# Optimization experiments

Measured on AMD Instinct MI355X. Metric: run time of the kernel, lower is better.

The kernel has to match this reference:

```python
import jax, jax.numpy as jnp
import numpy as np

B, D, N, H, K = 8192, 1024, 4096, 8, 4
T, DECAY, STEPS = 100.0, 0.001, 3


def setup_inputs() -> dict:
    key = jax.random.key(0)
    ks = jax.random.split(key, 16)
    rn = lambda k, sh, s=0.02: jax.random.normal(k, sh, jnp.float32) * s
    return {
        'query': jax.random.normal(ks[0], (B, D), jnp.float32),
        'wm': jax.random.normal(ks[1], (B, D), jnp.float32),
        'keys': jax.random.normal(ks[2], (N, D), jnp.float32) * 0.1,
        'values': jax.random.normal(ks[3], (N, D), jnp.float32) * 0.1,
        'last_access': jax.random.uniform(ks[4], (N,), jnp.float32) * T,
        'importance': jnp.ones((N,), jnp.float32),
        'consolid': jnp.ones((N,), jnp.float32),
        'emo_tags': jax.random.uniform(ks[5], (N, 8), jnp.float32),
        'active': jnp.ones((N,), jnp.float32),
        'in_proj_w': rn(ks[6], (3 * D, D)), 'in_proj_b': jnp.zeros((3 * D,), jnp.float32),
        'out_w': rn(ks[7], (D, D)), 'out_b': jnp.zeros((D,), jnp.float32),
        'msg_w1': rn(ks[8], (D, 2 * D)), 'msg_b1': jnp.zeros((D,), jnp.float32),
        'msg_ln_g': jnp.ones((D,), jnp.float32), 'msg_ln_b': jnp.zeros((D,), jnp.float32),
        'msg_w2': rn(ks[9], (D, D)), 'msg_b2': jnp.zeros((D,), jnp.float32),
        'gru_wih': rn(ks[10], (3 * D, D)), 'gru_whh': rn(ks[11], (3 * D, D)),
        'gru_bih': jnp.zeros((3 * D,), jnp.float32), 'gru_bhh': jnp.zeros((3 * D,), jnp.float32),
        'rsn_w1': rn(ks[12], (D, D)), 'rsn_b1': jnp.zeros((D,), jnp.float32),
        'rsn_ln_g': jnp.ones((D,), jnp.float32), 'rsn_ln_b': jnp.zeros((D,), jnp.float32),
        'rsn_w2': rn(ks[13], (D, D)), 'rsn_b2': jnp.zeros((D,), jnp.float32),
        'top_k': K,
    }


def _ln(x, g, b):
    m = x.mean(-1, keepdims=True)
    v = ((x - m) ** 2).mean(-1, keepdims=True)
    return (x - m) / jnp.sqrt(v + 1e-5) * g + b


def reference(query, wm, keys, values, last_access, importance, consolid, emo_tags, active,
              in_proj_w, in_proj_b, out_w, out_b,
              msg_w1, msg_b1, msg_ln_g, msg_ln_b, msg_w2, msg_b2,
              gru_wih, gru_whh, gru_bih, gru_bhh,
              rsn_w1, rsn_b1, rsn_ln_g, rsn_ln_b, rsn_w2, rsn_b2, top_k):
    sg = jax.lax.stop_gradient
    # --- schema retrieve: cosine sim + forgetting-decay + boosts + topk softmax gather ---
    qn = query / jnp.maximum(jnp.linalg.norm(query, axis=-1, keepdims=True), 1e-8)
    kn = keys / jnp.maximum(jnp.linalg.norm(keys, axis=-1, keepdims=True), 1e-8)
    sims = qn @ kn.T  # [B, N]
    forget = sg(jnp.exp(-DECAY * (T - last_access)))
    boost = sg(emo_tags.sum(-1) * 0.1 + importance * 0.2 + jnp.log1p(consolid) * 0.1)
    scores = (sims * forget + boost) * sg(active)
    top_s, top_i = jax.lax.top_k(scores, top_k)  # [B, K]
    w = jax.nn.softmax(top_s, axis=-1)
    schema = jnp.einsum('bk,bkd->bd', w, values[top_i])  # [B, D]

    # --- GraphReasoner: 3 steps of 2-token MHA + msg_net + GRUCell ---
    dh = D // H
    scale = 1.0 / np.sqrt(dh).astype(np.float32)

    def mha(x):  # x [B, 2, D]
        qkv = x @ in_proj_w.T + in_proj_b
        q, k, v = jnp.split(qkv, 3, axis=-1)
        q = q.reshape(-1, 2, H, dh); k = k.reshape(-1, 2, H, dh); v = v.reshape(-1, 2, H, dh)
        a = jax.nn.softmax(jnp.einsum('bqhd,bkhd->bhqk', q, k) * scale, axis=-1)
        o = jnp.einsum('bhqk,bkhd->bqhd', a, v).reshape(-1, 2, D)
        return o @ out_w.T + out_b

    def gru(x, h):
        gi = x @ gru_wih.T + gru_bih
        gh = h @ gru_whh.T + gru_bhh
        ir, iz, inn = jnp.split(gi, 3, axis=-1)
        hr, hz, hn = jnp.split(gh, 3, axis=-1)
        r = jax.nn.sigmoid(ir + hr)
        z = jax.nn.sigmoid(iz + hz)
        n = jnp.tanh(inn + r * hn)
        return (1.0 - z) * n + z * h

    state = wm
    for _ in range(STEPS):
        ctx = jnp.stack([state, schema], axis=1)  # [B, 2, D]
        att = mha(ctx)
        combined = jnp.concatenate([att[:, 0], att[:, 1]], axis=-1)  # [B, 2D]
        msg = jax.nn.relu(_ln(combined @ msg_w1.T + msg_b1, msg_ln_g, msg_ln_b)) @ msg_w2.T + msg_b2
        state = gru(msg, state)
    out = jax.nn.relu(_ln(state @ rsn_w1.T + rsn_b1, rsn_ln_g, rsn_ln_b)) @ rsn_w2.T + rsn_b2
    return out
```

## Files before the change

### kernel.cpp

```cpp
#include <hip/hip_runtime.h>
#include <cstdint>
#include <cstddef>

typedef __attribute__((ext_vector_type(8))) short short8;
typedef __attribute__((ext_vector_type(4))) float f32x4;
typedef __attribute__((ext_vector_type(4))) unsigned short us4;

#define DEVINL static __device__ __forceinline__
#define AS1 __attribute__((address_space(1)))
#define AS3 __attribute__((address_space(3)))

DEVINL float bf2f(unsigned short u){
  union { unsigned uu; float f; } v; v.uu = ((unsigned)u) << 16; return v.f;
}
DEVINL unsigned short f2bf(float f){
  unsigned u = __float_as_uint(f);
  u += 0x7fffu + ((u >> 16) & 1u);
  return (unsigned short)(u >> 16);
}

DEVINL bool tk_better(float av, int ai, float bv, int bi){
  return (av > bv) || (av == bv && ai < bi);
}
DEVINL void tk_cmpex(float& va, int& ia, float& vb, int& ib){
  if (!tk_better(va, ia, vb, ib)){
    float tv = va; va = vb; vb = tv;
    int t = ia; ia = ib; ib = t;
  }
}
DEVINL void tk_sort4(float* v, int* id){
  tk_cmpex(v[0], id[0], v[1], id[1]);
  tk_cmpex(v[2], id[2], v[3], id[3]);
  tk_cmpex(v[0], id[0], v[2], id[2]);
  tk_cmpex(v[1], id[1], v[3], id[3]);
  tk_cmpex(v[1], id[1], v[2], id[2]);
}
DEVINL void tk_bmerge(float* v, int* id, const float* pv, const int* pi){
  #pragma unroll
  for (int i = 0; i < 4; ++i){
    bool ta = tk_better(v[i], id[i], pv[3 - i], pi[3 - i]);
    v[i]  = ta ? v[i]  : pv[3 - i];
    id[i] = ta ? id[i] : pi[3 - i];
  }
  tk_cmpex(v[0], id[0], v[2], id[2]);
  tk_cmpex(v[1], id[1], v[3], id[3]);
  tk_cmpex(v[0], id[0], v[1], id[1]);
  tk_cmpex(v[2], id[2], v[3], id[3]);
}

__global__ void k_diag(float* out, float v){ out[0] = v; }

__global__ __launch_bounds__(256) void k_cast_bf16(const float* __restrict__ x,
                                                   unsigned short* __restrict__ y, int n4){
  int stride = gridDim.x * blockDim.x;
  for (int i = blockIdx.x * blockDim.x + threadIdx.x; i < n4; i += stride){
    float4 v = ((const float4*)x)[i];
    us4 o; o[0] = f2bf(v.x); o[1] = f2bf(v.y); o[2] = f2bf(v.z); o[3] = f2bf(v.w);
    ((us4*)y)[i] = o;
  }
}

__global__ __launch_bounds__(256) void k_tcast(const float* __restrict__ in,
    unsigned short* __restrict__ outT, int R, int C){
  __shared__ float t[32][33];
  const int bc = blockIdx.x * 32, br = blockIdx.y * 32;
  const int lx = threadIdx.x & 31, ly = threadIdx.x >> 5;
  #pragma unroll
  for (int i = 0; i < 32; i += 8)
    t[ly + i][lx] = in[(size_t)(br + ly + i) * C + bc + lx];
  __syncthreads();
  #pragma unroll
  for (int i = 0; i < 32; i += 8)
    outT[(size_t)(bc + ly + i) * R + br + lx] = f2bf(t[lx][ly + i]);
}

__global__ __launch_bounds__(256) void k_bias_pre(const float* __restrict__ w1,
    const float* __restrict__ outb, const float* __restrict__ b1, float* __restrict__ bc){
  int wave = threadIdx.x >> 6, lane = threadIdx.x & 63;
  int j = blockIdx.x * 4 + wave;
  float s = 0.f;
  for (int m = lane; m < 2048; m += 64)
    s += w1[(size_t)j * 2048 + m] * outb[m & 1023];
  #pragma unroll
  for (int m = 32; m >= 1; m >>= 1) s += __shfl_xor(s, m);
  if (lane == 0) bc[j] = s + b1[j];
}

__global__ __launch_bounds__(256) void k_bias_gi(const float* __restrict__ wih,
    const float* __restrict__ b2, const float* __restrict__ bih, float* __restrict__ bc){
  int wave = threadIdx.x >> 6, lane = threadIdx.x & 63;
  int n = blockIdx.x * 4 + wave;
  float s = 0.f;
  for (int m = lane; m < 1024; m += 64)
    s += wih[(size_t)n * 1024 + m] * b2[m];
  #pragma unroll
  for (int m = 32; m >= 1; m >>= 1) s += __shfl_xor(s, m);
  if (lane == 0) bc[n] = s + bih[n];
}

__global__ __launch_bounds__(256) void k_prep_keys(const float* __restrict__ keys,
    const float* __restrict__ last_access, const float* __restrict__ importance,
    const float* __restrict__ consolid, const float* __restrict__ emo,
    const float* __restrict__ active, float* __restrict__ ascale, float* __restrict__ bbias){
  int wave = threadIdx.x >> 6, lane = threadIdx.x & 63;
  int n = blockIdx.x * 4 + wave;
  const float* kr = keys + (size_t)n * 1024;
  float s = 0.f;
  #pragma unroll
  for (int j = 0; j < 4; ++j){
    float4 v = ((const float4*)kr)[j * 64 + lane];
    s += v.x*v.x + v.y*v.y + v.z*v.z + v.w*v.w;
  }
  #pragma unroll
  for (int m = 32; m >= 1; m >>= 1) s += __shfl_xor(s, m);
  if (lane == 0){
    float norm = fmaxf(sqrtf(s), 1e-8f);
    float forget = expf(-0.001f * (100.0f - last_access[n]));
    float bo = 0.f;
    #pragma unroll
    for (int j = 0; j < 8; ++j) bo += emo[n * 8 + j];
    bo = bo * 0.1f + importance[n] * 0.2f + log1pf(consolid[n]) * 0.1f;
    float a = active[n];
    ascale[n] = forget * a / norm;
    bbias[n]  = bo * a;
  }
}

__global__ __launch_bounds__(256) void k_qnorm(const float* __restrict__ q, float* __restrict__ qinv){
  int wave = threadIdx.x >> 6, lane = threadIdx.x & 63;
  int b = blockIdx.x * 4 + wave;
  const float* qr = q + (size_t)b * 1024;
  float s = 0.f;
  #pragma unroll
  for (int j = 0; j < 4; ++j){
    float4 v = ((const float4*)qr)[j * 64 + lane];
    s += v.x*v.x + v.y*v.y + v.z*v.z + v.w*v.w;
  }
  #pragma unroll
  for (int m = 32; m >= 1; m >>= 1) s += __shfl_xor(s, m);
  if (lane == 0) qinv[b] = 1.0f / fmaxf(sqrtf(s), 1e-8f);
}

__global__ __launch_bounds__(256) void k_split(const float* __restrict__ X,
    const float* __restrict__ rscale, unsigned short* __restrict__ Hi,
    unsigned short* __restrict__ Lo){
  const int row = blockIdx.x;
  const float sc = rscale ? rscale[row] : 1.0f;
  const int d = threadIdx.x * 4;
  float4 v = *(const float4*)(X + (size_t)row * 1024 + d);
  float xs[4] = {v.x * sc, v.y * sc, v.z * sc, v.w * sc};
  us4 h, l;
  #pragma unroll
  for (int j = 0; j < 4; ++j){
    unsigned short hb = f2bf(xs[j]);
    h[j] = hb;
    l[j] = f2bf(xs[j] - bf2f(hb));
  }
  *(us4*)(Hi + (size_t)row * 1024 + d) = h;
  *(us4*)(Lo + (size_t)row * 1024 + d) = l;
}

__global__ __launch_bounds__(256) void k_scores_mfma(
    const unsigned short* __restrict__ Qhi, const unsigned short* __restrict__ Qlo,
    const unsigned short* __restrict__ Khi, const unsigned short* __restrict__ Klo,
    const float* __restrict__ ascale, const float* __restrict__ bbias,
    float* __restrict__ candV, int* __restrict__ candI){
  __shared__ __align__(16) unsigned short AsH[128 * 32];
  __shared__ __align__(16) unsigned short AsL[128 * 32];
  __shared__ __align__(16) unsigned short BsH[128 * 32];
  __shared__ __align__(16) unsigned short BsL[128 * 32];
  const int tid = threadIdx.x;
  const int wave = tid >> 6, lane = tid & 63;
  const int tM = blockIdx.x, tN = blockIdx.y;
  const int wm_ = wave >> 1, wn_ = wave & 1;
  f32x4 acc[4][4] = {};
  const unsigned short* AH = Qhi + (size_t)tM * 128 * 1024;
  const unsigned short* AL = Qlo + (size_t)tM * 128 * 1024;
  const unsigned short* BH = Khi + (size_t)tN * 128 * 1024;
  const unsigned short* BL = Klo + (size_t)tN * 128 * 1024;
  const int lrow = lane & 15, lk = (lane >> 4) * 8;
  for (int k0 = 0; k0 < 1024; k0 += 32){
    __syncthreads();
    #pragma unroll
    for (int j = 0; j < 2; ++j){
      int c = wave * 128 + j * 64 + lane;
      int row = c >> 2, cp = c & 3;
      size_t go = (size_t)row * 1024 + k0 + cp * 8;
      int lo_ = (wave * 2 + j) * 512;
      __builtin_amdgcn_global_load_lds((const AS1 void*)(AH + go), (AS3 void*)(AsH + lo_), 16, 0, 0);
      __builtin_amdgcn_global_load_lds((const AS1 void*)(AL + go), (AS3 void*)(AsL + lo_), 16, 0, 0);
      __builtin_amdgcn_global_load_lds((const AS1 void*)(BH + go), (AS3 void*)(BsH + lo_), 16, 0, 0);
      __builtin_amdgcn_global_load_lds((const AS1 void*)(BL + go), (AS3 void*)(BsL + lo_), 16, 0, 0);
    }
    __syncthreads();
    short8 ah[4], al[4], bh[4], bl[4];
    #pragma unroll
    for (int mi = 0; mi < 4; ++mi){
      int ro = (wm_ * 64 + mi * 16 + lrow) * 32 + lk;
      ah[mi] = *(const short8*)(AsH + ro);
      al[mi] = *(const short8*)(AsL + ro);
    }
    #pragma unroll
    for (int ni = 0; ni < 4; ++ni){
      int ro = (wn_ * 64 + ni * 16 + lrow) * 32 + lk;
      bh[ni] = *(const short8*)(BsH + ro);
      bl[ni] = *(const short8*)(BsL + ro);
    }
    #pragma unroll
    for (int mi = 0; mi < 4; ++mi)
      #pragma unroll
      for (int ni = 0; ni < 4; ++ni){
        acc[mi][ni] = __builtin_amdgcn_mfma_f32_16x16x32_bf16(ah[mi], bh[ni], acc[mi][ni], 0, 0, 0);
        acc[mi][ni] = __builtin_amdgcn_mfma_f32_16x16x32_bf16(ah[mi], bl[ni], acc[mi][ni], 0, 0, 0);
        acc[mi][ni] = __builtin_amdgcn_mfma_f32_16x16x32_bf16(al[mi], bh[ni], acc[mi][ni], 0, 0, 0);
      }
  }
  const int lc = lane & 15;
  float as_[4], bb_[4]; int cid[4];
  #pragma unroll
  for (int ni = 0; ni < 4; ++ni){
    cid[ni] = tN * 128 + wn_ * 64 + ni * 16 + lc;
    as_[ni] = ascale[cid[ni]];
    bb_[ni] = bbias[cid[ni]];
  }
  #pragma unroll
  for (int mi = 0; mi < 4; ++mi){
    #pragma unroll
    for (int r = 0; r < 4; ++r){
      float v[4]; int id[4];
      #pragma unroll
      for (int ni = 0; ni < 4; ++ni){
        v[ni]  = acc[mi][ni][r] * as_[ni] + bb_[ni];
        id[ni] = cid[ni];
      }
      tk_sort4(v, id);
      #pragma unroll
      for (int mask = 1; mask <= 8; mask <<= 1){
        float pv[4]; int pi_[4];
        #pragma unroll
        for (int j = 0; j < 4; ++j){
          pv[j]  = __shfl_xor(v[j], mask);
          pi_[j] = __shfl_xor(id[j], mask);
        }
        tk_bmerge(v, id, pv, pi_);
      }
      if (lc == 0){
        int row = tM * 128 + wm_ * 64 + mi * 16 + (lane >> 4) * 4 + r;
        size_t cb = (size_t)row * 256 + tN * 8 + wn_ * 4;
        #pragma unroll
        for (int j = 0; j < 4; ++j){ candV[cb + j] = v[j]; candI[cb + j] = id[j]; }
      }
    }
  }
}

__global__ __launch_bounds__(256) void k_topk_merge(const float* __restrict__ candV,
    const int* __restrict__ candI, const float* __restrict__ V,
    unsigned short* __restrict__ schema_bf){
  const int row = blockIdx.x, tid = threadIdx.x;
  const int wave = tid >> 6, lane = tid & 63;
  float v[4]; int id[4];
  v[0] = candV[(size_t)row * 256 + tid];
  id[0] = candI[(size_t)row * 256 + tid];
  #pragma unroll
  for (int j = 1; j < 4; ++j){ v[j] = -3.4e38f; id[j] = 0x7fffffff; }
  #pragma unroll
  for (int mask = 1; mask <= 32; mask <<= 1){
    float pv[4]; int pi_[4];
    #pragma unroll
    for (int j = 0; j < 4; ++j){
      pv[j]  = __shfl_xor(v[j], mask);
      pi_[j] = __shfl_xor(id[j], mask);
    }
    tk_bmerge(v, id, pv, pi_);
  }
  __shared__ float wv[4][4]; __shared__ int wi[4][4];
  if (lane == 0){
    #pragma unroll
    for (int j = 0; j < 4; ++j){ wv[wave][j] = v[j]; wi[wave][j] = id[j]; }
  }
  __syncthreads();
  __shared__ float w_sh[4]; __shared__ int i_sh[4];
  if (tid == 0){
    float fv[4]; int fi[4];
    #pragma unroll
    for (int j = 0; j < 4; ++j){ fv[j] = wv[0][j]; fi[j] = wi[0][j]; }
    #pragma unroll
    for (int w = 1; w < 4; ++w){
      float pv[4]; int pi_[4];
      #pragma unroll
      for (int j = 0; j < 4; ++j){ pv[j] = wv[w][j]; pi_[j] = wi[w][j]; }
      tk_bmerge(fv, fi, pv, pi_);
    }
    float m = fv[0];
    float e0 = expf(fv[0] - m), e1 = expf(fv[1] - m), e2 = expf(fv[2] - m), e3 = expf(fv[3] - m);
    float inv = 1.f / (e0 + e1 + e2 + e3);
    w_sh[0] = e0 * inv; w_sh[1] = e1 * inv; w_sh[2] = e2 * inv; w_sh[3] = e3 * inv;
    i_sh[0] = fi[0]; i_sh[1] = fi[1]; i_sh[2] = fi[2]; i_sh[3] = fi[3];
  }
  __syncthreads();
  float w0 = w_sh[0], w1 = w_sh[1], w2 = w_sh[2], w3 = w_sh[3];
  const float* v0 = V + (size_t)i_sh[0] * 1024;
  const float* v1 = V + (size_t)i_sh[1] * 1024;
  const float* v2 = V + (size_t)i_sh[2] * 1024;
  const float* v3 = V + (size_t)i_sh[3] * 1024;
  int d = tid * 4;
  float4 a = *(const float4*)(v0 + d);
  float4 b4 = *(const float4*)(v1 + d);
  float4 c = *(const float4*)(v2 + d);
  float4 e = *(const float4*)(v3 + d);
  us4 o;
  o[0] = f2bf(w0*a.x + w1*b4.x + w2*c.x + w3*e.x);
  o[1] = f2bf(w0*a.y + w1*b4.y + w2*c.y + w3*e.y);
  o[2] = f2bf(w0*a.z + w1*b4.z + w2*c.z + w3*e.z);
  o[3] = f2bf(w0*a.w + w1*b4.w + w2*c.w + w3*e.w);
  *(us4*)(schema_bf + (size_t)row * 1024 + d) = o;
}

__global__ __launch_bounds__(256) void k_initstate(const float* __restrict__ wm,
    float* __restrict__ st, unsigned short* __restrict__ stbf){
  size_t i = ((size_t)blockIdx.x * 256 + threadIdx.x) * 4;
  float4 v = *(const float4*)(wm + i);
  *(float4*)(st + i) = v;
  us4 o; o[0] = f2bf(v.x); o[1] = f2bf(v.y); o[2] = f2bf(v.z); o[3] = f2bf(v.w);
  *(us4*)(stbf + i) = o;
}

template<int OUT_BF16>
__global__ __launch_bounds__(256) void k_gemm(const unsigned short* __restrict__ A,
    const unsigned short* __restrict__ W, const float* __restrict__ bias,
    void* __restrict__ C, int M, int N, int K, int lda, int ldc){
  __shared__ __align__(16) unsigned short As[128 * 32];
  __shared__ __align__(16) unsigned short Ws[128 * 32];
  const int tid = threadIdx.x;
  const int wave = tid >> 6, lane = tid & 63;
  const int tM = blockIdx.x, tN = blockIdx.y;
  const int wm_ = wave >> 1, wn_ = wave & 1;
  f32x4 acc[4][4] = {};
  const unsigned short* Abase = A + (size_t)tM * 128 * lda;
  const unsigned short* Wbase = W + (size_t)tN * 128 * K;
  const int lrow = lane & 15, lk = (lane >> 4) * 8;
  for (int k0 = 0; k0 < K; k0 += 32){
    __syncthreads();
    #pragma unroll
    for (int j = 0; j < 2; ++j){
      int c = wave * 128 + j * 64 + lane;
      int row = c >> 2, cp = c & 3;
      const unsigned short* ga = Abase + (size_t)row * lda + k0 + cp * 8;
      const unsigned short* gw = Wbase + (size_t)row * K + k0 + cp * 8;
      __builtin_amdgcn_global_load_lds((const AS1 void*)ga, (AS3 void*)(As + (wave * 2 + j) * 512), 16, 0, 0);
      __builtin_amdgcn_global_load_lds((const AS1 void*)gw, (AS3 void*)(Ws + (wave * 2 + j) * 512), 16, 0, 0);
    }
    __syncthreads();
    short8 af[4], bfr[4];
    #pragma unroll
    for (int mi = 0; mi < 4; ++mi)
      af[mi] = *(const short8*)(As + (wm_ * 64 + mi * 16 + lrow) * 32 + lk);
    #pragma unroll
    for (int ni = 0; ni < 4; ++ni)
      bfr[ni] = *(const short8*)(Ws + (wn_ * 64 + ni * 16 + lrow) * 32 + lk);
    #pragma unroll
    for (int mi = 0; mi < 4; ++mi)
      #pragma unroll
      for (int ni = 0; ni < 4; ++ni)
        acc[mi][ni] = __builtin_amdgcn_mfma_f32_16x16x32_bf16(af[mi], bfr[ni], acc[mi][ni], 0, 0, 0);
  }
  const int lc = lane & 15, lr = (lane >> 4) * 4;
  #pragma unroll
  for (int ni = 0; ni < 4; ++ni){
    int col = tN * 128 + wn_ * 64 + ni * 16 + lc;
    float bb = bias ? bias[col] : 0.f;
    #pragma unroll
    for (int mi = 0; mi < 4; ++mi){
      int rowb = tM * 128 + wm_ * 64 + mi * 16 + lr;
      #pragma unroll
      for (int r = 0; r < 4; ++r){
        float vv = acc[mi][ni][r] + bb;
        size_t off = (size_t)(rowb + r) * ldc + col;
        if (OUT_BF16) ((unsigned short*)C)[off] = f2bf(vv);
        else ((float*)C)[off] = vv;
      }
    }
  }
}

template<int OUT_BF16>
__global__ __launch_bounds__(512, 2) void k_gemm8p(const unsigned short* __restrict__ A,
    const unsigned short* __restrict__ W, const float* __restrict__ bias,
    void* __restrict__ C, int M, int N, int K, int lda, int ldc){
  __shared__ __align__(16) unsigned short lds[65536];
  const int tid = threadIdx.x;
  const int wave = tid >> 6, lane = tid & 63;
  const int wqr = wave >> 2, wqc = wave & 3;
  const int lrow = lane & 15, lkk = lane >> 4;

  const int nwg = gridDim.x * gridDim.y;
  int lin = blockIdx.y * gridDim.x + blockIdx.x;
  int cpx = nwg >> 3;
  int swz = (lin & 7) * cpx + (lin >> 3);
  const int nM = M >> 8;
  const int tM = swz % nM, tN = swz / nM;

  const unsigned short* Abase = A + (size_t)tM * 256 * lda;
  const unsigned short* Wbase = W + (size_t)tN * 256 * K;

  f32x4 a00[4][2] = {}, a01[4][2] = {}, a11[4][2] = {}, a10[4][2] = {};
  short8 af[4][2], bf[2][2];
  const int ntiles = K >> 6;

  auto stage = [&](int op, int slot, int half, int tile){
    if (tile >= ntiles) return;
    const unsigned short* G = op ? Wbase : Abase;
    const int rs = op ? K : lda;
    const int k0 = tile * 64, hr = half * 128;
    const int base = op * 32768 + slot * 16384 + half * 8192;
    #pragma unroll
    for (int l = 0; l < 2; ++l){
      int p = l * 512 + tid;
      int row = p >> 3, c = (p & 7) ^ (row & 7);
      int dstc = l * 512 + wave * 64;
      __builtin_amdgcn_global_load_lds(
          (const AS1 void*)(G + (size_t)(hr + row) * rs + k0 + c * 8),
          (AS3 void*)(lds + base + dstc * 8), 16, 0, 0);
    }
  };
  auto ldA = [&](int slot, int half){
    const int base = slot * 16384 + half * 8192;
    #pragma unroll
    for (int mi = 0; mi < 4; ++mi)
      #pragma unroll
      for (int kk = 0; kk < 2; ++kk){
        int row = wqr * 64 + mi * 16 + lrow;
        int c = kk * 4 + lkk;
        af[mi][kk] = *(const short8*)(lds + base + (row * 8 + (c ^ (row & 7))) * 8);
      }
  };
  auto ldB = [&](int slot, int half){
    const int base = 32768 + slot * 16384 + half * 8192;
    #pragma unroll
    for (int ni = 0; ni < 2; ++ni)
      #pragma unroll
      for (int kk = 0; kk < 2; ++kk){
        int row = wqc * 32 + ni * 16 + lrow;
        int c = kk * 4 + lkk;
        bf[ni][kk] = *(const short8*)(lds + base + (row * 8 + (c ^ (row & 7))) * 8);
      }
  };
  auto mfma16 = [&](f32x4 (&acc)[4][2]){
    __builtin_amdgcn_s_setprio(1);
    #pragma unroll
    for (int mi = 0; mi < 4; ++mi)
      #pragma unroll
      for (int ni = 0; ni < 2; ++ni)
        #pragma unroll
        for (int kk = 0; kk < 2; ++kk)
          acc[mi][ni] = __builtin_amdgcn_mfma_f32_16x16x32_bf16(af[mi][kk], bf[ni][kk], acc[mi][ni], 0, 0, 0);
    __builtin_amdgcn_s_setprio(0);
  };
  auto SB = [&](){
    __builtin_amdgcn_sched_barrier(0);
    __builtin_amdgcn_s_barrier();
    __builtin_amdgcn_sched_barrier(0);
  };

  stage(0,0,0, 0); stage(1,0,0, 0); stage(1,0,1, 0); stage(0,0,1, 0);
  stage(0,1,0, 1); stage(1,1,1, 1);
  __builtin_amdgcn_sched_barrier(0);
  asm volatile("s_waitcnt vmcnt(4)" ::: "memory");
  __builtin_amdgcn_s_barrier();
  __builtin_amdgcn_sched_barrier(0);

  for (int j = 0; j < (ntiles >> 1); ++j){
    const int t0 = 2 * j;
    ldA(0,0); ldB(0,0); stage(0,1,1, t0+1);
    SB(); mfma16(a00); SB();
    ldB(0,1); stage(1,1,0, t0+1);
    SB(); mfma16(a01); SB();
    ldA(0,1); stage(0,0,0, t0+2);
    SB(); mfma16(a11); SB();
    ldB(0,0); stage(1,0,1, t0+2);
    SB(); mfma16(a10);
    __builtin_amdgcn_sched_barrier(0);
    if (t0 + 2 < ntiles) asm volatile("s_waitcnt vmcnt(4)" ::: "memory");
    else                 asm volatile("s_waitcnt vmcnt(0)" ::: "memory");
    __builtin_amdgcn_s_barrier();
    __builtin_amdgcn_sched_barrier(0);
    ldA(1,0); ldB(1,0); stage(0,0,1, t0+2);
    SB(); mfma16(a00); SB();
    ldB(1,1); stage(1,0,0, t0+2);
    SB(); mfma16(a01); SB();
    ldA(1,1); stage(0,1,0, t0+3);
    SB(); mfma16(a11); SB();
    ldB(1,0); stage(1,1,1, t0+3);
    SB(); mfma16(a10);
    __builtin_amdgcn_sched_barrier(0);
    asm volatile("s_waitcnt vmcnt(4)" ::: "memory");
    __builtin_amdgcn_s_barrier();
    __builtin_amdgcn_sched_barrier(0);
  }

  const int lc = lane & 15, lr = (lane >> 4) * 4;
  auto wout = [&](f32x4 (&acc)[4][2], int MH, int NH){
    #pragma unroll
    for (int ni = 0; ni < 2; ++ni){
      int col = tN * 256 + NH * 128 + wqc * 32 + ni * 16 + lc;
      float bb = bias ? bias[col] : 0.f;
      #pragma unroll
      for (int mi = 0; mi < 4; ++mi){
        int rowb = tM * 256 + MH * 128 + wqr * 64 + mi * 16 + lr;
        #pragma unroll
        for (int r = 0; r < 4; ++r){
          float vv = acc[mi][ni][r] + bb;
          size_t off = (size_t)(rowb + r) * ldc + col;
          if (OUT_BF16) ((unsigned short*)C)[off] = f2bf(vv);
          else ((float*)C)[off] = vv;
        }
      }
    }
  };
  wout(a00, 0, 0); wout(a01, 0, 1); wout(a11, 1, 1); wout(a10, 1, 0);
}

__global__ __launch_bounds__(256) void k_attn(const unsigned short* __restrict__ qkvS,
    const unsigned short* __restrict__ qkvM, unsigned short* __restrict__ catt){
  const int b = blockIdx.x, tid = threadIdx.x;
  const int l = tid & 31;
  const int e = (tid >> 5) * 128 + l * 4;
  const unsigned short* ps = qkvS + (size_t)b * 3072;
  const unsigned short* pm = qkvM + (size_t)b * 3072;
  float q0[4], kk0[4], v0[4], q1[4], kk1[4], v1[4];
  us4 t;
  t = *(const us4*)(ps + e);        for (int j = 0; j < 4; ++j) q0[j]  = bf2f(t[j]);
  t = *(const us4*)(ps + 1024 + e); for (int j = 0; j < 4; ++j) kk0[j] = bf2f(t[j]);
  t = *(const us4*)(ps + 2048 + e); for (int j = 0; j < 4; ++j) v0[j]  = bf2f(t[j]);
  t = *(const us4*)(pm + e);        for (int j = 0; j < 4; ++j) q1[j]  = bf2f(t[j]);
  t = *(const us4*)(pm + 1024 + e); for (int j = 0; j < 4; ++j) kk1[j] = bf2f(t[j]);
  t = *(const us4*)(pm + 2048 + e); for (int j = 0; j < 4; ++j) v1[j]  = bf2f(t[j]);
  float s00 = 0.f, s01 = 0.f, s10 = 0.f, s11 = 0.f;
  #pragma unroll
  for (int j = 0; j < 4; ++j){
    s00 += q0[j] * kk0[j]; s01 += q0[j] * kk1[j];
    s10 += q1[j] * kk0[j]; s11 += q1[j] * kk1[j];
  }
  #pragma unroll
  for (int m = 16; m >= 1; m >>= 1){
    s00 += __shfl_xor(s00, m); s01 += __shfl_xor(s01, m);
    s10 += __shfl_xor(s10, m); s11 += __shfl_xor(s11, m);
  }
  const float sc = 0.08838834764831845f;
  s00 *= sc; s01 *= sc; s10 *= sc; s11 *= sc;
  float m0 = fmaxf(s00, s01), m1 = fmaxf(s10, s11);
  float e00 = expf(s00 - m0), e01 = expf(s01 - m0);
  float e10 = expf(s10 - m1), e11 = expf(s11 - m1);
  float i0 = 1.f / (e00 + e01), i1 = 1.f / (e10 + e11);
  float w00 = e00 * i0, w01 = e01 * i0, w10 = e10 * i1, w11 = e11 * i1;
  us4 o0, o1;
  #pragma unroll
  for (int j = 0; j < 4; ++j){
    o0[j] = f2bf(w00 * v0[j] + w01 * v1[j]);
    o1[j] = f2bf(w10 * v0[j] + w11 * v1[j]);
  }
  *(us4*)(catt + (size_t)b * 2048 + e)        = o0;
  *(us4*)(catt + (size_t)b * 2048 + 1024 + e) = o1;
}

__global__ __launch_bounds__(256) void k_ln_relu(const float* __restrict__ X,
    const float* __restrict__ g, const float* __restrict__ bta, unsigned short* __restrict__ Y){
  const int row = blockIdx.x, tid = threadIdx.x;
  const float* x = X + (size_t)row * 1024;
  const int d = tid * 4;
  float4 v = *(const float4*)(x + d);
  float s1 = v.x + v.y + v.z + v.w;
  float s2 = v.x*v.x + v.y*v.y + v.z*v.z + v.w*v.w;
  #pragma unroll
  for (int m = 32; m >= 1; m >>= 1){ s1 += __shfl_xor(s1, m); s2 += __shfl_xor(s2, m); }
  __shared__ float a1[4], a2[4];
  int wave = tid >> 6, lane = tid & 63;
  if (lane == 0){ a1[wave] = s1; a2[wave] = s2; }
  __syncthreads();
  s1 = a1[0] + a1[1] + a1[2] + a1[3];
  s2 = a2[0] + a2[1] + a2[2] + a2[3];
  float mean = s1 * (1.f / 1024.f);
  float var  = s2 * (1.f / 1024.f) - mean * mean;
  float rstd = rsqrtf(var + 1e-5f);
  float4 gg = *(const float4*)(g + d);
  float4 bb = *(const float4*)(bta + d);
  us4 o;
  o[0] = f2bf(fmaxf((v.x - mean) * rstd * gg.x + bb.x, 0.f));
  o[1] = f2bf(fmaxf((v.y - mean) * rstd * gg.y + bb.y, 0.f));
  o[2] = f2bf(fmaxf((v.z - mean) * rstd * gg.z + bb.z, 0.f));
  o[3] = f2bf(fmaxf((v.w - mean) * rstd * gg.w + bb.w, 0.f));
  *(us4*)(Y + (size_t)row * 1024 + d) = o;
}

__global__ __launch_bounds__(256) void k_gru(const unsigned short* __restrict__ gi,
    const unsigned short* __restrict__ gh, const float* __restrict__ h,
    float* __restrict__ hn, unsigned short* __restrict__ hnbf){
  const int b = blockIdx.x;
  const int d = threadIdx.x * 4;
  const unsigned short* pi = gi + (size_t)b * 3072;
  const unsigned short* ph = gh + (size_t)b * 3072;
  us4 t;
  float ir[4], iz[4], in_[4], hr[4], hz[4], hnn[4];
  t = *(const us4*)(pi + d);        for (int j = 0; j < 4; ++j) ir[j]  = bf2f(t[j]);
  t = *(const us4*)(pi + 1024 + d); for (int j = 0; j < 4; ++j) iz[j]  = bf2f(t[j]);
  t = *(const us4*)(pi + 2048 + d); for (int j = 0; j < 4; ++j) in_[j] = bf2f(t[j]);
  t = *(const us4*)(ph + d);        for (int j = 0; j < 4; ++j) hr[j]  = bf2f(t[j]);
  t = *(const us4*)(ph + 1024 + d); for (int j = 0; j < 4; ++j) hz[j]  = bf2f(t[j]);
  t = *(const us4*)(ph + 2048 + d); for (int j = 0; j < 4; ++j) hnn[j] = bf2f(t[j]);
  float4 hv = *(const float4*)(h + (size_t)b * 1024 + d);
  float hvv[4] = {hv.x, hv.y, hv.z, hv.w};
  float ov[4]; us4 ob;
  #pragma unroll
  for (int j = 0; j < 4; ++j){
    float r = 1.f / (1.f + expf(-(ir[j] + hr[j])));
    float z = 1.f / (1.f + expf(-(iz[j] + hz[j])));
    float n = tanhf(in_[j] + r * hnn[j]);
    float o = (1.f - z) * n + z * hvv[j];
    ov[j] = o; ob[j] = f2bf(o);
  }
  float4 of; of.x = ov[0]; of.y = ov[1]; of.z = ov[2]; of.w = ov[3];
  *(float4*)(hn + (size_t)b * 1024 + d) = of;
  *(us4*)(hnbf + (size_t)b * 1024 + d) = ob;
}

extern "C" void kernel_launch(void* const* d_in, const int* in_sizes, int n_in,
                              void* d_out, int out_size, void* d_ws, size_t ws_size,
                              hipStream_t stream) {
  (void)in_sizes; (void)n_in; (void)out_size;
  const float* query       = (const float*)d_in[0];
  const float* wm          = (const float*)d_in[1];
  const float* keys        = (const float*)d_in[2];
  const float* values      = (const float*)d_in[3];
  const float* last_access = (const float*)d_in[4];
  const float* importance  = (const float*)d_in[5];
  const float* consolid    = (const float*)d_in[6];
  const float* emo         = (const float*)d_in[7];
  const float* active      = (const float*)d_in[8];
  const float* in_proj_w   = (const float*)d_in[9];
  const float* in_proj_b   = (const float*)d_in[10];
  const float* out_w       = (const float*)d_in[11];
  const float* out_b       = (const float*)d_in[12];
  const float* msg_w1      = (const float*)d_in[13];
  const float* msg_b1      = (const float*)d_in[14];
  const float* msg_ln_g    = (const float*)d_in[15];
  const float* msg_ln_b    = (const float*)d_in[16];
  const float* msg_w2      = (const float*)d_in[17];
  const float* msg_b2      = (const float*)d_in[18];
  const float* gru_wih     = (const float*)d_in[19];
  const float* gru_whh     = (const float*)d_in[20];
  const float* gru_bih     = (const float*)d_in[21];
  const float* gru_bhh     = (const float*)d_in[22];
  const float* rsn_w1      = (const float*)d_in[23];
  const float* rsn_b1      = (const float*)d_in[24];
  const float* rsn_ln_g    = (const float*)d_in[25];
  const float* rsn_ln_b    = (const float*)d_in[26];
  const float* rsn_w2      = (const float*)d_in[27];
  const float* rsn_b2      = (const float*)d_in[28];
  float* out = (float*)d_out;

  size_t off = 0;
  char* base = (char*)d_ws;
  auto carve = [&](size_t bytes) -> char* {
    char* p = base + off;
    off += (bytes + 255) & ~(size_t)255;
    return p;
  };
  float* ascale = (float*)carve(4096*4);
  float* bbias  = (float*)carve(4096*4);
  float* qinv   = (float*)carve(8192*4);
  float* bc_pre = (float*)carve(1024*4);
  float* bc_gi  = (float*)carve(3072*4);
  unsigned short* wb_inproj = (unsigned short*)carve((size_t)3072*1024*2);
  unsigned short* wb_gwhh   = (unsigned short*)carve((size_t)3072*1024*2);
  unsigned short* wb_rw1    = (unsigned short*)carve((size_t)1024*1024*2);
  unsigned short* wb_rw2    = (unsigned short*)carve((size_t)1024*1024*2);
  unsigned short* wb_Wab    = (unsigned short*)carve((size_t)1024*2048*2);
  unsigned short* wb_Wc     = (unsigned short*)carve((size_t)3072*1024*2);
  unsigned short* schema_bf = (unsigned short*)carve((size_t)8192*1024*2);
  float*          state_f   = (float*)carve((size_t)8192*1024*4);
  unsigned short* state_bf  = (unsigned short*)carve((size_t)8192*1024*2);
  unsigned short* qkvM      = (unsigned short*)carve((size_t)8192*3072*2);
  unsigned short* bufP      = (unsigned short*)carve((size_t)8192*3072*2);
  unsigned short* bufQ      = (unsigned short*)carve((size_t)8192*3072*2);

  if (off > ws_size){
    k_diag<<<1, 1, 0, stream>>>(out, (float)(ws_size >> 20));
    return;
  }

  unsigned short* tmp_w1bf  = bufQ;
  unsigned short* tmp_outwT = bufQ + (size_t)1024*2048;
  unsigned short* tmp_w2T   = tmp_outwT + (size_t)1024*1024;
  unsigned short* tmp_wihbf = tmp_w2T + (size_t)1024*1024;

  unsigned short* Qhi = qkvM;
  unsigned short* Qlo = Qhi + (size_t)8192*1024;
  unsigned short* Khi = Qlo + (size_t)8192*1024;
  unsigned short* Klo = Khi + (size_t)4096*1024;
  float* candV = (float*)bufP;
  int*   candI = (int*)((char*)bufP + (size_t)8192*256*4);

  unsigned short* qkvS  = bufP;
  unsigned short* catt  = bufQ;
  float*          preln = (float*)bufP;
  unsigned short* h1buf = bufQ;
  unsigned short* gibuf = bufP;
  unsigned short* ghbuf = bufQ;

  auto cast = [&](const float* src, unsigned short* dst, int n){
    k_cast_bf16<<<1024, 256, 0, stream>>>(src, dst, n / 4);
  };
  cast(in_proj_w, wb_inproj, 3072*1024);
  cast(gru_whh,   wb_gwhh,   3072*1024);
  cast(rsn_w1,    wb_rw1,    1024*1024);
  cast(rsn_w2,    wb_rw2,    1024*1024);
  cast(msg_w1,    tmp_w1bf,  1024*2048);
  cast(gru_wih,   tmp_wihbf, 3072*1024);
  k_tcast<<<dim3(32, 32), 256, 0, stream>>>(out_w,  tmp_outwT, 1024, 1024);
  k_tcast<<<dim3(32, 32), 256, 0, stream>>>(msg_w2, tmp_w2T,   1024, 1024);
  k_bias_pre<<<256, 256, 0, stream>>>(msg_w1, out_b, msg_b1, bc_pre);
  k_bias_gi<<<768, 256, 0, stream>>>(gru_wih, msg_b2, gru_bih, bc_gi);
  k_gemm<1><<<dim3(8, 8), 256, 0, stream>>>(tmp_w1bf,        tmp_outwT, nullptr, wb_Wab,        1024, 1024, 1024, 2048, 2048);
  k_gemm<1><<<dim3(8, 8), 256, 0, stream>>>(tmp_w1bf + 1024, tmp_outwT, nullptr, wb_Wab + 1024, 1024, 1024, 1024, 2048, 2048);
  k_gemm<1><<<dim3(24, 8), 256, 0, stream>>>(tmp_wihbf, tmp_w2T, nullptr, wb_Wc, 3072, 1024, 1024, 1024, 1024);

  k_qnorm<<<2048, 256, 0, stream>>>(query, qinv);
  k_prep_keys<<<1024, 256, 0, stream>>>(keys, last_access, importance, consolid, emo, active, ascale, bbias);
  k_split<<<8192, 256, 0, stream>>>(query, qinv, Qhi, Qlo);
  k_split<<<4096, 256, 0, stream>>>(keys, nullptr, Khi, Klo);
  k_scores_mfma<<<dim3(64, 32), 256, 0, stream>>>(Qhi, Qlo, Khi, Klo, ascale, bbias, candV, candI);
  k_topk_merge<<<8192, 256, 0, stream>>>(candV, candI, values, schema_bf);

  k_initstate<<<8192, 256, 0, stream>>>(wm, state_f, state_bf);
  k_gemm8p<1><<<dim3(32, 12), 512, 0, stream>>>(schema_bf, wb_inproj, in_proj_b, qkvM, 8192, 3072, 1024, 1024, 3072);
  for (int s = 0; s < 3; ++s){
    k_gemm8p<1><<<dim3(32, 12), 512, 0, stream>>>(state_bf, wb_inproj, in_proj_b, qkvS, 8192, 3072, 1024, 1024, 3072);
    k_attn<<<8192, 256, 0, stream>>>(qkvS, qkvM, catt);
    k_gemm<0><<<dim3(64, 8), 256, 0, stream>>>(catt, wb_Wab, bc_pre, preln, 8192, 1024, 2048, 2048, 1024);
    k_ln_relu<<<8192, 256, 0, stream>>>(preln, msg_ln_g, msg_ln_b, h1buf);
    k_gemm8p<1><<<dim3(32, 12), 512, 0, stream>>>(h1buf, wb_Wc, bc_gi, gibuf, 8192, 3072, 1024, 1024, 3072);
    k_gemm8p<1><<<dim3(32, 12), 512, 0, stream>>>(state_bf, wb_gwhh, gru_bhh, ghbuf, 8192, 3072, 1024, 1024, 3072);
    k_gru<<<8192, 256, 0, stream>>>(gibuf, ghbuf, state_f, state_f, state_bf);
  }
  k_gemm<0><<<dim3(64, 8), 256, 0, stream>>>(state_bf, wb_rw1, rsn_b1, (float*)bufP, 8192, 1024, 1024, 1024, 1024);
  k_ln_relu<<<8192, 256, 0, stream>>>((float*)bufP, rsn_ln_g, rsn_ln_b, bufQ);
  k_gemm<0><<<dim3(64, 8), 256, 0, stream>>>(bufQ, wb_rw2, rsn_b2, out, 8192, 1024, 1024, 1024, 1024);
}
```

Measured before the change: 1.564 ms.

## Replace 256x256 GEMM with 256x128 triple-buffered kernel and swizzle scores LDS

After: 1.627 ms. +4.0%, slower.

```diff
diff --git a/kernel.cpp b/kernel.cpp
--- a/kernel.cpp
+++ b/kernel.cpp
@@ -178,13 +178,13 @@
   const unsigned short* AL = Qlo + (size_t)tM * 128 * 1024;
   const unsigned short* BH = Khi + (size_t)tN * 128 * 1024;
   const unsigned short* BL = Klo + (size_t)tN * 128 * 1024;
-  const int lrow = lane & 15, lk = (lane >> 4) * 8;
+  const int lrow = lane & 15, cc = lane >> 4;
   for (int k0 = 0; k0 < 1024; k0 += 32){
     __syncthreads();
     #pragma unroll
     for (int j = 0; j < 2; ++j){
       int c = wave * 128 + j * 64 + lane;
-      int row = c >> 2, cp = c & 3;
+      int row = c >> 2, cp = (c & 3) ^ (row & 3);
       size_t go = (size_t)row * 1024 + k0 + cp * 8;
       int lo_ = (wave * 2 + j) * 512;
       __builtin_amdgcn_global_load_lds((const AS1 void*)(AH + go), (AS3 void*)(AsH + lo_), 16, 0, 0);
@@ -196,13 +196,15 @@
     short8 ah[4], al[4], bh[4], bl[4];
     #pragma unroll
     for (int mi = 0; mi < 4; ++mi){
-      int ro = (wm_ * 64 + mi * 16 + lrow) * 32 + lk;
+      int rA = wm_ * 64 + mi * 16 + lrow;
+      int ro = rA * 32 + ((cc ^ (rA & 3)) * 8);
       ah[mi] = *(const short8*)(AsH + ro);
       al[mi] = *(const short8*)(AsL + ro);
     }
     #pragma unroll
     for (int ni = 0; ni < 4; ++ni){
-      int ro = (wn_ * 64 + ni * 16 + lrow) * 32 + lk;
+      int rB = wn_ * 64 + ni * 16 + lrow;
+      int ro = rB * 32 + ((cc ^ (rB & 3)) * 8);
       bh[ni] = *(const short8*)(BsH + ro);
       bl[ni] = *(const short8*)(BsL + ro);
     }
@@ -385,10 +387,10 @@
 }
 
 template<int OUT_BF16>
-__global__ __launch_bounds__(512, 2) void k_gemm8p(const unsigned short* __restrict__ A,
+__global__ __launch_bounds__(512, 1) void k_gtall(const unsigned short* __restrict__ A,
     const unsigned short* __restrict__ W, const float* __restrict__ bias,
     void* __restrict__ C, int M, int N, int K, int lda, int ldc){
-  __shared__ __align__(16) unsigned short lds[65536];
+  __shared__ __align__(16) unsigned short lds[73728];
   const int tid = threadIdx.x;
   const int wave = tid >> 6, lane = tid & 63;
   const int wqr = wave >> 2, wqc = wave & 3;
@@ -402,30 +404,38 @@
   const int tM = swz % nM, tN = swz / nM;
 
   const unsigned short* Abase = A + (size_t)tM * 256 * lda;
-  const unsigned short* Wbase = W + (size_t)tN * 256 * K;
-
-  f32x4 a00[4][2] = {}, a01[4][2] = {}, a11[4][2] = {}, a10[4][2] = {};
+  const unsigned short* Wbase = W + (size_t)tN * 128 * K;
+
+  f32x4 a0[4][2] = {}, a1[4][2] = {};
   short8 af[4][2], bf[2][2];
   const int ntiles = K >> 6;
 
-  auto stage = [&](int op, int slot, int half, int tile){
-    if (tile >= ntiles) return;
-    const unsigned short* G = op ? Wbase : Abase;
-    const int rs = op ? K : lda;
+  auto stageA = [&](int half, int tile, int slot){
     const int k0 = tile * 64, hr = half * 128;
-    const int base = op * 32768 + slot * 16384 + half * 8192;
+    const int base = slot * 24576 + half * 8192;
     #pragma unroll
     for (int l = 0; l < 2; ++l){
       int p = l * 512 + tid;
       int row = p >> 3, c = (p & 7) ^ (row & 7);
-      int dstc = l * 512 + wave * 64;
       __builtin_amdgcn_global_load_lds(
-          (const AS1 void*)(G + (size_t)(hr + row) * rs + k0 + c * 8),
-          (AS3 void*)(lds + base + dstc * 8), 16, 0, 0);
+          (const AS1 void*)(Abase + (size_t)(hr + row) * lda + k0 + c * 8),
+          (AS3 void*)(lds + base + (l * 512 + wave * 64) * 8), 16, 0, 0);
+    }
+  };
+  auto stageB = [&](int tile, int slot){
+    const int k0 = tile * 64;
+    const int base = slot * 24576 + 16384;
+    #pragma unroll
+    for (int l = 0; l < 2; ++l){
+      int p = l * 512 + tid;
+      int row = p >> 3, c = (p & 7) ^ (row & 7);
+      __builtin_amdgcn_global_load_lds(
+          (const AS1 void*)(Wbase + (size_t)row * K + k0 + c * 8),
+          (AS3 void*)(lds + base + (l * 512 + wave * 64) * 8), 16, 0, 0);
     }
   };
   auto ldA = [&](int slot, int half){
-    const int base = slot * 16384 + half * 8192;
+    const int base = slot * 24576 + half * 8192;
     #pragma unroll
     for (int mi = 0; mi < 4; ++mi)
       #pragma unroll
@@ -435,8 +445,8 @@
         af[mi][kk] = *(const short8*)(lds + base + (row * 8 + (c ^ (row & 7))) * 8);
       }
   };
-  auto ldB = [&](int slot, int half){
-    const int base = 32768 + slot * 16384 + half * 8192;
+  auto ldB = [&](int slot){
+    const int base = slot * 24576 + 16384;
     #pragma unroll
     for (int ni = 0; ni < 2; ++ni)
       #pragma unroll
@@ -463,47 +473,36 @@
     __builtin_amdgcn_sched_barrier(0);
   };
 
-  stage(0,0,0, 0); stage(1,0,0, 0); stage(1,0,1, 0); stage(0,0,1, 0);
-  stage(0,1,0, 1); stage(1,1,1, 1);
+  stageA(0, 0, 0); stageA(1, 0, 0); stageB(0, 0);
+  stageA(0, 1, 1); stageA(1, 1, 1); stageB(1, 1);
   __builtin_amdgcn_sched_barrier(0);
-  asm volatile("s_waitcnt vmcnt(4)" ::: "memory");
+  asm volatile("s_waitcnt vmcnt(6)" ::: "memory");
   __builtin_amdgcn_s_barrier();
   __builtin_amdgcn_sched_barrier(0);
 
-  for (int j = 0; j < (ntiles >> 1); ++j){
-    const int t0 = 2 * j;
-    ldA(0,0); ldB(0,0); stage(0,1,1, t0+1);
-    SB(); mfma16(a00); SB();
-    ldB(0,1); stage(1,1,0, t0+1);
-    SB(); mfma16(a01); SB();
-    ldA(0,1); stage(0,0,0, t0+2);
-    SB(); mfma16(a11); SB();
-    ldB(0,0); stage(1,0,1, t0+2);
-    SB(); mfma16(a10);
+  int slot = 0;
+  for (int t = 0; t < ntiles; ++t){
+    int s2 = slot + 2; if (s2 >= 3) s2 -= 3;
+    const bool pf = (t + 2 < ntiles);
+    ldA(slot, 0); ldB(slot);
+    if (pf){ stageA(0, t + 2, s2); stageA(1, t + 2, s2); }
+    SB(); mfma16(a0); SB();
+    ldA(slot, 1);
+    if (pf){ stageB(t + 2, s2); }
+    SB(); mfma16(a1);
     __builtin_amdgcn_sched_barrier(0);
-    if (t0 + 2 < ntiles) asm volatile("s_waitcnt vmcnt(4)" ::: "memory");
-    else                 asm volatile("s_waitcnt vmcnt(0)" ::: "memory");
+    if (pf) asm volatile("s_waitcnt vmcnt(6)" ::: "memory");
+    else    asm volatile("s_waitcnt vmcnt(0)" ::: "memory");
     __builtin_amdgcn_s_barrier();
     __builtin_amdgcn_sched_barrier(0);
-    ldA(1,0); ldB(1,0); stage(0,0,1, t0+2);
-    SB(); mfma16(a00); SB();
-    ldB(1,1); stage(1,0,0, t0+2);
-    SB(); mfma16(a01); SB();
-    ldA(1,1); stage(0,1,0, t0+3);
-    SB(); mfma16(a11); SB();
-    ldB(1,0); stage(1,1,1, t0+3);
-    SB(); mfma16(a10);
-    __builtin_amdgcn_sched_barrier(0);
-    asm volatile("s_waitcnt vmcnt(4)" ::: "memory");
-    __builtin_amdgcn_s_barrier();
-    __builtin_amdgcn_sched_barrier(0);
+    slot = (slot + 1 == 3) ? 0 : slot + 1;
   }
 
   const int lc = lane & 15, lr = (lane >> 4) * 4;
-  auto wout = [&](f32x4 (&acc)[4][2], int MH, int NH){
+  auto wout = [&](f32x4 (&acc)[4][2], int MH){
     #pragma unroll
     for (int ni = 0; ni < 2; ++ni){
-      int col = tN * 256 + NH * 128 + wqc * 32 + ni * 16 + lc;
+      int col = tN * 128 + wqc * 32 + ni * 16 + lc;
       float bb = bias ? bias[col] : 0.f;
       #pragma unroll
       for (int mi = 0; mi < 4; ++mi){
@@ -518,7 +517,7 @@
       }
     }
   };
-  wout(a00, 0, 0); wout(a01, 0, 1); wout(a11, 1, 1); wout(a10, 1, 0);
+  wout(a0, 0); wout(a1, 1);
 }
 
 __global__ __launch_bounds__(256) void k_attn(const unsigned short* __restrict__ qkvS,
@@ -733,17 +732,17 @@
   k_topk_merge<<<8192, 256, 0, stream>>>(candV, candI, values, schema_bf);
 
   k_initstate<<<8192, 256, 0, stream>>>(wm, state_f, state_bf);
-  k_gemm8p<1><<<dim3(32, 12), 512, 0, stream>>>(schema_bf, wb_inproj, in_proj_b, qkvM, 8192, 3072, 1024, 1024, 3072);
+  k_gtall<1><<<dim3(32, 24), 512, 0, stream>>>(schema_bf, wb_inproj, in_proj_b, qkvM, 8192, 3072, 1024, 1024, 3072);
   for (int s = 0; s < 3; ++s){
-    k_gemm8p<1><<<dim3(32, 12), 512, 0, stream>>>(state_bf, wb_inproj, in_proj_b, qkvS, 8192, 3072, 1024, 1024, 3072);
+    k_gtall<1><<<dim3(32, 24), 512, 0, stream>>>(state_bf, wb_inproj, in_proj_b, qkvS, 8192, 3072, 1024, 1024, 3072);
     k_attn<<<8192, 256, 0, stream>>>(qkvS, qkvM, catt);
-    k_gemm<0><<<dim3(64, 8), 256, 0, stream>>>(catt, wb_Wab, bc_pre, preln, 8192, 1024, 2048, 2048, 1024);
+    k_gtall<0><<<dim3(32, 8), 512, 0, stream>>>(catt, wb_Wab, bc_pre, preln, 8192, 1024, 2048, 2048, 1024);
     k_ln_relu<<<8192, 256, 0, stream>>>(preln, msg_ln_g, msg_ln_b, h1buf);
-    k_gemm8p<1><<<dim3(32, 12), 512, 0, stream>>>(h1buf, wb_Wc, bc_gi, gibuf, 8192, 3072, 1024, 1024, 3072);
-    k_gemm8p<1><<<dim3(32, 12), 512, 0, stream>>>(state_bf, wb_gwhh, gru_bhh, ghbuf, 8192, 3072, 1024, 1024, 3072);
+    k_gtall<1><<<dim3(32, 24), 512, 0, stream>>>(h1buf, wb_Wc, bc_gi, gibuf, 8192, 3072, 1024, 1024, 3072);
+    k_gtall<1><<<dim3(32, 24), 512, 0, stream>>>(state_bf, wb_gwhh, gru_bhh, ghbuf, 8192, 3072, 1024, 1024, 3072);
     k_gru<<<8192, 256, 0, stream>>>(gibuf, ghbuf, state_f, state_f, state_bf);
   }
-  k_gemm<0><<<dim3(64, 8), 256, 0, stream>>>(state_bf, wb_rw1, rsn_b1, (float*)bufP, 8192, 1024, 1024, 1024, 1024);
+  k_gtall<0><<<dim3(32, 8), 512, 0, stream>>>(state_bf, wb_rw1, rsn_b1, (float*)bufP, 8192, 1024, 1024, 1024, 1024);
   k_ln_relu<<<8192, 256, 0, stream>>>((float*)bufP, rsn_ln_g, rsn_ln_b, bufQ);
-  k_gemm<0><<<dim3(64, 8), 256, 0, stream>>>(bufQ, wb_rw2, rsn_b2, out, 8192, 1024, 1024, 1024, 1024);
-}
+  k_gtall<0><<<dim3(32, 8), 512, 0, stream>>>(bufQ, wb_rw2, rsn_b2, out, 8192, 1024, 1024, 1024, 1024);
+}
```

## Merge state in-proj and GRU hidden GEMMs into one wide GEMM with bf16 intermediates

Applied to the files above, without the earlier changes.

Result: faster. 1.502 ms (-3.9%).

```diff
diff --git a/kernel.cpp b/kernel.cpp
--- a/kernel.cpp
+++ b/kernel.cpp
@@ -521,12 +521,12 @@
   wout(a00, 0, 0); wout(a01, 0, 1); wout(a11, 1, 1); wout(a10, 1, 0);
 }
 
-__global__ __launch_bounds__(256) void k_attn(const unsigned short* __restrict__ qkvS,
-    const unsigned short* __restrict__ qkvM, unsigned short* __restrict__ catt){
+__global__ __launch_bounds__(256) void k_attn(unsigned short* qgh,
+    const unsigned short* __restrict__ qkvM){
   const int b = blockIdx.x, tid = threadIdx.x;
   const int l = tid & 31;
   const int e = (tid >> 5) * 128 + l * 4;
-  const unsigned short* ps = qkvS + (size_t)b * 3072;
+  unsigned short* ps = qgh + (size_t)b * 6144;
   const unsigned short* pm = qkvM + (size_t)b * 3072;
   float q0[4], kk0[4], v0[4], q1[4], kk1[4], v1[4];
   us4 t;
@@ -560,18 +560,25 @@
     o0[j] = f2bf(w00 * v0[j] + w01 * v1[j]);
     o1[j] = f2bf(w10 * v0[j] + w11 * v1[j]);
   }
-  *(us4*)(catt + (size_t)b * 2048 + e)        = o0;
-  *(us4*)(catt + (size_t)b * 2048 + 1024 + e) = o1;
-}
-
-__global__ __launch_bounds__(256) void k_ln_relu(const float* __restrict__ X,
-    const float* __restrict__ g, const float* __restrict__ bta, unsigned short* __restrict__ Y){
+  *(us4*)(ps + e)        = o0;
+  *(us4*)(ps + 1024 + e) = o1;
+}
+
+template<int IN_BF16>
+__global__ __launch_bounds__(256) void k_ln_relu(const void* X,
+    const float* __restrict__ g, const float* __restrict__ bta, unsigned short* Y){
   const int row = blockIdx.x, tid = threadIdx.x;
-  const float* x = X + (size_t)row * 1024;
   const int d = tid * 4;
-  float4 v = *(const float4*)(x + d);
-  float s1 = v.x + v.y + v.z + v.w;
-  float s2 = v.x*v.x + v.y*v.y + v.z*v.z + v.w*v.w;
+  float e0, e1, e2, e3;
+  if (IN_BF16){
+    us4 t = *(const us4*)((const unsigned short*)X + (size_t)row * 1024 + d);
+    e0 = bf2f(t[0]); e1 = bf2f(t[1]); e2 = bf2f(t[2]); e3 = bf2f(t[3]);
+  } else {
+    float4 v = *(const float4*)((const float*)X + (size_t)row * 1024 + d);
+    e0 = v.x; e1 = v.y; e2 = v.z; e3 = v.w;
+  }
+  float s1 = e0 + e1 + e2 + e3;
+  float s2 = e0*e0 + e1*e1 + e2*e2 + e3*e3;
   #pragma unroll
   for (int m = 32; m >= 1; m >>= 1){ s1 += __shfl_xor(s1, m); s2 += __shfl_xor(s2, m); }
   __shared__ float a1[4], a2[4];
@@ -586,20 +593,19 @@
   float4 gg = *(const float4*)(g + d);
   float4 bb = *(const float4*)(bta + d);
   us4 o;
-  o[0] = f2bf(fmaxf((v.x - mean) * rstd * gg.x + bb.x, 0.f));
-  o[1] = f2bf(fmaxf((v.y - mean) * rstd * gg.y + bb.y, 0.f));
-  o[2] = f2bf(fmaxf((v.z - mean) * rstd * gg.z + bb.z, 0.f));
-  o[3] = f2bf(fmaxf((v.w - mean) * rstd * gg.w + bb.w, 0.f));
+  o[0] = f2bf(fmaxf((e0 - mean) * rstd * gg.x + bb.x, 0.f));
+  o[1] = f2bf(fmaxf((e1 - mean) * rstd * gg.y + bb.y, 0.f));
+  o[2] = f2bf(fmaxf((e2 - mean) * rstd * gg.z + bb.z, 0.f));
+  o[3] = f2bf(fmaxf((e3 - mean) * rstd * gg.w + bb.w, 0.f));
   *(us4*)(Y + (size_t)row * 1024 + d) = o;
 }
 
-__global__ __launch_bounds__(256) void k_gru(const unsigned short* __restrict__ gi,
-    const unsigned short* __restrict__ gh, const float* __restrict__ h,
-    float* __restrict__ hn, unsigned short* __restrict__ hnbf){
+__global__ __launch_bounds__(256) void k_gru(const unsigned short* __restrict__ qgh,
+    const float* __restrict__ h, float* __restrict__ hn, unsigned short* __restrict__ hnbf){
   const int b = blockIdx.x;
   const int d = threadIdx.x * 4;
-  const unsigned short* pi = gi + (size_t)b * 3072;
-  const unsigned short* ph = gh + (size_t)b * 3072;
+  const unsigned short* pi = qgh + (size_t)b * 6144;
+  const unsigned short* ph = pi + 3072;
   us4 t;
   float ir[4], iz[4], in_[4], hr[4], hz[4], hnn[4];
   t = *(const us4*)(pi + d);        for (int j = 0; j < 4; ++j) ir[j]  = bf2f(t[j]);
@@ -671,26 +677,25 @@
   float* qinv   = (float*)carve(8192*4);
   float* bc_pre = (float*)carve(1024*4);
   float* bc_gi  = (float*)carve(3072*4);
-  unsigned short* wb_inproj = (unsigned short*)carve((size_t)3072*1024*2);
-  unsigned short* wb_gwhh   = (unsigned short*)carve((size_t)3072*1024*2);
-  unsigned short* wb_rw1    = (unsigned short*)carve((size_t)1024*1024*2);
-  unsigned short* wb_rw2    = (unsigned short*)carve((size_t)1024*1024*2);
-  unsigned short* wb_Wab    = (unsigned short*)carve((size_t)1024*2048*2);
-  unsigned short* wb_Wc     = (unsigned short*)carve((size_t)3072*1024*2);
+  float* bc_ih  = (float*)carve(6144*4);
+  unsigned short* wb_ihh  = (unsigned short*)carve((size_t)6144*1024*2);
+  unsigned short* wb_rw1  = (unsigned short*)carve((size_t)1024*1024*2);
+  unsigned short* wb_rw2  = (unsigned short*)carve((size_t)1024*1024*2);
+  unsigned short* wb_Wab  = (unsigned short*)carve((size_t)1024*2048*2);
+  unsigned short* wb_Wc   = (unsigned short*)carve((size_t)3072*1024*2);
   unsigned short* schema_bf = (unsigned short*)carve((size_t)8192*1024*2);
   float*          state_f   = (float*)carve((size_t)8192*1024*4);
   unsigned short* state_bf  = (unsigned short*)carve((size_t)8192*1024*2);
   unsigned short* qkvM      = (unsigned short*)carve((size_t)8192*3072*2);
-  unsigned short* bufP      = (unsigned short*)carve((size_t)8192*3072*2);
-  unsigned short* bufQ      = (unsigned short*)carve((size_t)8192*3072*2);
+  unsigned short* qgh       = (unsigned short*)carve((size_t)8192*6144*2);
 
   if (off > ws_size){
     k_diag<<<1, 1, 0, stream>>>(out, (float)(ws_size >> 20));
     return;
   }
 
-  unsigned short* tmp_w1bf  = bufQ;
-  unsigned short* tmp_outwT = bufQ + (size_t)1024*2048;
+  unsigned short* tmp_w1bf  = qgh;
+  unsigned short* tmp_outwT = qgh + (size_t)1024*2048;
   unsigned short* tmp_w2T   = tmp_outwT + (size_t)1024*1024;
   unsigned short* tmp_wihbf = tmp_w2T + (size_t)1024*1024;
 
@@ -698,25 +703,22 @@
   unsigned short* Qlo = Qhi + (size_t)8192*1024;
   unsigned short* Khi = Qlo + (size_t)8192*1024;
   unsigned short* Klo = Khi + (size_t)4096*1024;
-  float* candV = (float*)bufP;
-  int*   candI = (int*)((char*)bufP + (size_t)8192*256*4);
-
-  unsigned short* qkvS  = bufP;
-  unsigned short* catt  = bufQ;
-  float*          preln = (float*)bufP;
-  unsigned short* h1buf = bufQ;
-  unsigned short* gibuf = bufP;
-  unsigned short* ghbuf = bufQ;
+  float* candV = (float*)(qgh + (size_t)8192*3072);
+  int*   candI = (int*)((char*)candV + (size_t)8192*256*4);
+
+  unsigned short* preln_h1 = schema_bf;
 
   auto cast = [&](const float* src, unsigned short* dst, int n){
     k_cast_bf16<<<1024, 256, 0, stream>>>(src, dst, n / 4);
   };
-  cast(in_proj_w, wb_inproj, 3072*1024);
-  cast(gru_whh,   wb_gwhh,   3072*1024);
+  cast(in_proj_w, wb_ihh,                     3072*1024);
+  cast(gru_whh,   wb_ihh + (size_t)3072*1024, 3072*1024);
   cast(rsn_w1,    wb_rw1,    1024*1024);
   cast(rsn_w2,    wb_rw2,    1024*1024);
   cast(msg_w1,    tmp_w1bf,  1024*2048);
   cast(gru_wih,   tmp_wihbf, 3072*1024);
+  hipMemcpyAsync(bc_ih,        in_proj_b, 3072*4, hipMemcpyDeviceToDevice, stream);
+  hipMemcpyAsync(bc_ih + 3072, gru_bhh,   3072*4, hipMemcpyDeviceToDevice, stream);
   k_tcast<<<dim3(32, 32), 256, 0, stream>>>(out_w,  tmp_outwT, 1024, 1024);
   k_tcast<<<dim3(32, 32), 256, 0, stream>>>(msg_w2, tmp_w2T,   1024, 1024);
   k_bias_pre<<<256, 256, 0, stream>>>(msg_w1, out_b, msg_b1, bc_pre);
@@ -733,17 +735,18 @@
   k_topk_merge<<<8192, 256, 0, stream>>>(candV, candI, values, schema_bf);
 
   k_initstate<<<8192, 256, 0, stream>>>(wm, state_f, state_bf);
-  k_gemm8p<1><<<dim3(32, 12), 512, 0, stream>>>(schema_bf, wb_inproj, in_proj_b, qkvM, 8192, 3072, 1024, 1024, 3072);
+  k_gemm8p<1><<<dim3(32, 12), 512, 0, stream>>>(schema_bf, wb_ihh, bc_ih, qkvM, 8192, 3072, 1024, 1024, 3072);
   for (int s = 0; s < 3; ++s){
-    k_gemm8p<1><<<dim3(32, 12), 512, 0, stream>>>(state_bf, wb_inproj, in_proj_b, qkvS, 8192, 3072, 1024, 1024, 3072);
-    k_attn<<<8192, 256, 0, stream>>>(qkvS, qkvM, catt);
-    k_gemm<0><<<dim3(64, 8), 256, 0, stream>>>(catt, wb_Wab, bc_pre, preln, 8192, 1024, 2048, 2048, 1024);
-    k_ln_relu<<<8192, 256, 0, stream>>>(preln, msg_ln_g, msg_ln_b, h1buf);
-    k_gemm8p<1><<<dim3(32, 12), 512, 0, stream>>>(h1buf, wb_Wc, bc_gi, gibuf, 8192, 3072, 1024, 1024, 3072);
-    k_gemm8p<1><<<dim3(32, 12), 512, 0, stream>>>(state_bf, wb_gwhh, gru_bhh, ghbuf, 8192, 3072, 1024, 1024, 3072);
-    k_gru<<<8192, 256, 0, stream>>>(gibuf, ghbuf, state_f, state_f, state_bf);
-  }
-  k_gemm<0><<<dim3(64, 8), 256, 0, stream>>>(state_bf, wb_rw1, rsn_b1, (float*)bufP, 8192, 1024, 1024, 1024, 1024);
-  k_ln_relu<<<8192, 256, 0, stream>>>((float*)bufP, rsn_ln_g, rsn_ln_b, bufQ);
-  k_gemm<0><<<dim3(64, 8), 256, 0, stream>>>(bufQ, wb_rw2, rsn_b2, out, 8192, 1024, 1024, 1024, 1024);
-}
+    k_gemm8p<1><<<dim3(32, 24), 512, 0, stream>>>(state_bf, wb_ihh, bc_ih, qgh, 8192, 6144, 1024, 1024, 6144);
+    k_attn<<<8192, 256, 0, stream>>>(qgh, qkvM);
+    k_gemm<1><<<dim3(64, 8), 256, 0, stream>>>(qgh, wb_Wab, bc_pre, preln_h1, 8192, 1024, 2048, 6144, 1024);
+    k_ln_relu<1><<<8192, 256, 0, stream>>>(preln_h1, msg_ln_g, msg_ln_b, preln_h1);
+    k_gemm8p<1><<<dim3(32, 12), 512, 0, stream>>>(preln_h1, wb_Wc, bc_gi, qgh, 8192, 3072, 1024, 1024, 6144);
+    k_gru<<<8192, 256, 0, stream>>>(qgh, state_f, state_f, state_bf);
+  }
+  float* hpre = (float*)qgh;
+  unsigned short* hh1 = qgh + (size_t)8192*3072;
+  k_gemm<0><<<dim3(64, 8), 256, 0, stream>>>(state_bf, wb_rw1, rsn_b1, hpre, 8192, 1024, 1024, 1024, 1024);
+  k_ln_relu<0><<<8192, 256, 0, stream>>>(hpre, rsn_ln_g, rsn_ln_b, hh1);
+  k_gemm<0><<<dim3(64, 8), 256, 0, stream>>>(hh1, wb_rw2, rsn_b2, out, 8192, 1024, 1024, 1024, 1024);
+}
```
